# Performance work log

Measured on AMD Instinct MI355X. Metric: run time of the kernel, lower is better.

## Reference

```python
import jax, jax.numpy as jnp
import numpy as np

RADIUS = 8
EPS = 0.005

_DN = ('NCHW', 'OIHW', 'NCHW')

def _box_filter(t, r):
    """Separable normalized box filter with reflect padding. t: [H, W]."""
    ks = 2 * r + 1
    tp = jnp.pad(t, ((r, r), (r, r)), mode='reflect')[None, None]  # [1,1,H+2r,W+2r]
    kh = jnp.ones((1, 1, 1, ks), t.dtype) / ks
    kv = jnp.ones((1, 1, ks, 1), t.dtype) / ks
    out = jax.lax.conv_general_dilated(tp, kh, (1, 1), 'VALID', dimension_numbers=_DN)
    out = jax.lax.conv_general_dilated(out, kv, (1, 1), 'VALID', dimension_numbers=_DN)
    return out[0, 0]  # [H, W]

def setup_inputs() -> dict:
    key = jax.random.key(0)
    x = jax.random.uniform(key, (4096, 4096, 3), dtype=jnp.float32)
    return {"x": x}

def reference(x):
    # Rec.709 luma
    Y = 0.2126 * x[..., 0] + 0.7152 * x[..., 1] + 0.0722 * x[..., 2]  # [H,W]
    mean_I = _box_filter(Y, RADIUS)
    mean_II = _box_filter(Y * Y, RADIUS)
    var_I = mean_II - mean_I * mean_I
    a = var_I / (var_I + EPS)
    b = mean_I - a * mean_I
    mean_a = _box_filter(a, RADIUS)
    mean_b = _box_filter(b, RADIUS)
    Y_smooth = mean_a * Y + mean_b
    scale = (Y_smooth / jnp.maximum(Y, 1e-6))[..., None]  # [H,W,1]
    return jnp.clip(x * scale, 0.0, 1.0)
```

## Files before the change

### kernel.cpp

```cpp
#include <hip/hip_runtime.h>
#include <hip/hip_fp16.h>


#define HH 4096
#define WW 4096
#define TW 32
#define TH 64
#define SW 64
#define SH 96
#define SYS 65
#define HIS 49
#define HAS 33
#define INV289 (1.0f / 289.0f)
#define EPSV 0.005f

__device__ __forceinline__ int reflect_idx(int i, int n) {
    i = (i < 0) ? -i : i;
    i = (i >= n) ? (2 * n - 2 - i) : i;
    return i;
}

__global__ __launch_bounds__(256, 4) void gf_fused(const float* __restrict__ x,
                                                   float* __restrict__ out) {
    __shared__ __align__(16) char smem[15680 + 18816];
    __half*  sY    = (__half*)smem;
    __half2* ab    = (__half2*)smem;
    __half2* hIhII = (__half2*)(smem + 15680);
    __half2* hAhB  = (__half2*)(smem + 15680);

    const int t = threadIdx.x;
    const int tx = blockIdx.x * TW;
    const int ty = blockIdx.y * TH;

    {
        const int c  = t & 63;
        const int r0 = t >> 6;
        const bool interior = (tx >= 16) & (tx + 48 <= WW) & (ty >= 16) & (ty + 80 <= HH);
        if (interior) {
            const float* p = x + ((long)(ty + r0 - 16) * WW + (tx + c - 16)) * 3;
            for (int r = r0; r < SH; r += 4, p += 4 * WW * 3) {
                float Yv = 0.2126f * p[0] + 0.7152f * p[1] + 0.0722f * p[2];
                sY[r * SYS + c] = __float2half_rn(Yv);
            }
        } else {
            const int gx = reflect_idx(tx + c - 16, WW);
            for (int r = r0; r < SH; r += 4) {
                int gy = reflect_idx(ty + r - 16, HH);
                const float* p = x + ((long)gy * WW + gx) * 3;
                float Yv = 0.2126f * p[0] + 0.7152f * p[1] + 0.0722f * p[2];
                sY[r * SYS + c] = __float2half_rn(Yv);
            }
        }
    }
    __syncthreads();

    for (int task = t; task < SH * 3; task += 256) {
        int r = task % SH;
        int s = task / SH;
        int base = r * SYS + s * 16;
        int ob = r * HIS + s * 16;
        float sI = 0.f, sII = 0.f;
        #pragma unroll
        for (int k = 0; k <= 16; ++k) {
            float w = __half2float(sY[base + k]);
            sI += w; sII += w * w;
        }
        hIhII[ob] = __floats2half2_rn(sI, sII);
        #pragma unroll
        for (int j = 1; j < 16; ++j) {
            float va = __half2float(sY[base + 16 + j]);
            float vs = __half2float(sY[base + j - 1]);
            sI  += va - vs;
            sII += va * va - vs * vs;
            hIhII[ob + j] = __floats2half2_rn(sI, sII);
        }
    }
    __syncthreads();

    if (t < 240) {
        int c = t % 48;
        int q = t / 48;
        int r0 = q * 16;
        float sI = 0.f, sII = 0.f;
        #pragma unroll
        for (int k = 0; k <= 16; ++k) {
            float2 v = __half22float2(hIhII[(r0 + k) * HIS + c]);
            sI += v.x; sII += v.y;
        }
        #pragma unroll
        for (int j = 0; j < 16; ++j) {
            int o = r0 + j;
            float mI = sI * INV289;
            float mII = sII * INV289;
            float var = mII - mI * mI;
            float a = var / (var + EPSV);
            float b = mI - a * mI;
            ab[o * HIS + c] = __floats2half2_rn(a, b);
            if (j < 15) {
                float2 va = __half22float2(hIhII[(o + 17) * HIS + c]);
                float2 vs = __half22float2(hIhII[o * HIS + c]);
                sI  += va.x - vs.x;
                sII += va.y - vs.y;
            }
        }
    }
    __syncthreads();

    if (t < 160) {
        int r = t % 80;
        int s = t / 80;
        int base = r * HIS + s * 16;
        int ob = r * HAS + s * 16;
        float sA = 0.f, sB = 0.f;
        #pragma unroll
        for (int k = 0; k <= 16; ++k) {
            float2 v = __half22float2(ab[base + k]);
            sA += v.x; sB += v.y;
        }
        hAhB[ob] = __floats2half2_rn(sA, sB);
        #pragma unroll
        for (int j = 1; j < 16; ++j) {
            float2 va = __half22float2(ab[base + 16 + j]);
            float2 vs = __half22float2(ab[base + j - 1]);
            sA += va.x - vs.x;
            sB += va.y - vs.y;
            hAhB[ob + j] = __floats2half2_rn(sA, sB);
        }
    }
    __syncthreads();

    {
        int c = t & 31;
        int q = t >> 5;
        int r0 = q * 8;
        float sA = 0.f, sB = 0.f;
        #pragma unroll
        for (int k = 0; k <= 16; ++k) {
            float2 v = __half22float2(hAhB[(r0 + k) * HAS + c]);
            sA += v.x; sB += v.y;
        }
        #pragma unroll
        for (int j = 0; j < 8; ++j) {
            int o = r0 + j;
            float ma = sA * INV289;
            float mb = sB * INV289;
            int gy = ty + o, gx = tx + c;
            const float* p = x + ((long)gy * WW + gx) * 3;
            float rr = p[0], gg = p[1], bb = p[2];
            float Y = 0.2126f * rr + 0.7152f * gg + 0.0722f * bb;
            float scale = (ma * Y + mb) / fmaxf(Y, 1e-6f);
            float* qo = out + ((long)gy * WW + gx) * 3;
            qo[0] = fminf(fmaxf(rr * scale, 0.f), 1.f);
            qo[1] = fminf(fmaxf(gg * scale, 0.f), 1.f);
            qo[2] = fminf(fmaxf(bb * scale, 0.f), 1.f);
            if (j < 7) {
                float2 va = __half22float2(hAhB[(o + 17) * HAS + c]);
                float2 vs = __half22float2(hAhB[o * HAS + c]);
                sA += va.x - vs.x;
                sB += va.y - vs.y;
            }
        }
    }
}

extern "C" void kernel_launch(void* const* d_in, const int* in_sizes, int n_in,
                              void* d_out, int out_size, void* d_ws, size_t ws_size,
                              hipStream_t stream) {
    const float* x = (const float*)d_in[0];
    float* out = (float*)d_out;
    dim3 grid(WW / TW, HH / TH);
    gf_fused<<<grid, 256, 0, stream>>>(x, out);
}
```

Before: 397.2 us.

## Widen tiles to 64x64 with 512 threads, vectorize loads and stores

Doubles the tile width to 64 columns and the block size to 512 threads, which cuts the relative halo overhead (96x96 loaded per 64x64 output instead of 64x96 per 32x64). Global loads of RGB are vectorized as three float4 per four pixels. Output stores use float4 nontemporal stores, and two divisions are replaced with hardware reciprocal approximations. The cost is more shared memory per block and fewer blocks per CU, and the rcp approximation slightly changes numerics.

```diff
diff --git a/kernel.cpp b/kernel.cpp
--- a/kernel.cpp
+++ b/kernel.cpp
@@ -4,15 +4,20 @@
 
 #define HH 4096
 #define WW 4096
-#define TW 32
+#define TW 64
 #define TH 64
-#define SW 64
+#define SW 96
 #define SH 96
-#define SYS 65
-#define HIS 49
-#define HAS 33
+#define SYS 98
+#define HIS 81
+#define HAS 65
 #define INV289 (1.0f / 289.0f)
 #define EPSV 0.005f
+
+#define R1BYTES 25920
+#define R2BYTES 31104
+
+typedef float f32x4 __attribute__((ext_vector_type(4)));
 
 __device__ __forceinline__ int reflect_idx(int i, int n) {
     i = (i < 0) ? -i : i;
@@ -20,43 +25,55 @@
     return i;
 }
 
-__global__ __launch_bounds__(256, 4) void gf_fused(const float* __restrict__ x,
+__global__ __launch_bounds__(512, 4) void gf_fused(const float* __restrict__ x,
                                                    float* __restrict__ out) {
-    __shared__ __align__(16) char smem[15680 + 18816];
+    __shared__ __align__(16) char smem[R1BYTES + R2BYTES];
     __half*  sY    = (__half*)smem;
     __half2* ab    = (__half2*)smem;
-    __half2* hIhII = (__half2*)(smem + 15680);
-    __half2* hAhB  = (__half2*)(smem + 15680);
+    __half2* hIhII = (__half2*)(smem + R1BYTES);
+    __half2* hAhB  = (__half2*)(smem + R1BYTES);
 
     const int t = threadIdx.x;
     const int tx = blockIdx.x * TW;
     const int ty = blockIdx.y * TH;
 
     {
-        const int c  = t & 63;
-        const int r0 = t >> 6;
-        const bool interior = (tx >= 16) & (tx + 48 <= WW) & (ty >= 16) & (ty + 80 <= HH);
+        const bool interior = (tx >= 16) & (tx + SW - 16 <= WW) &
+                              (ty >= 16) & (ty + SH - 16 <= HH);
         if (interior) {
-            const float* p = x + ((long)(ty + r0 - 16) * WW + (tx + c - 16)) * 3;
-            for (int r = r0; r < SH; r += 4, p += 4 * WW * 3) {
-                float Yv = 0.2126f * p[0] + 0.7152f * p[1] + 0.0722f * p[2];
-                sY[r * SYS + c] = __float2half_rn(Yv);
+            for (int task = t; task < SH * 24; task += 512) {
+                int r = task / 24;
+                int g = task - r * 24;
+                const float4* p = (const float4*)(x + ((long)(ty + r - 16) * WW + (tx - 16 + 4 * g)) * 3);
+                float4 f0 = p[0], f1 = p[1], f2 = p[2];
+                float Y0 = 0.2126f * f0.x + 0.7152f * f0.y + 0.0722f * f0.z;
+                float Y1 = 0.2126f * f0.w + 0.7152f * f1.x + 0.0722f * f1.y;
+                float Y2 = 0.2126f * f1.z + 0.7152f * f1.w + 0.0722f * f2.x;
+                float Y3 = 0.2126f * f2.y + 0.7152f * f2.z + 0.0722f * f2.w;
+                __half2* q2 = (__half2*)&sY[r * SYS + 4 * g];
+                q2[0] = __floats2half2_rn(Y0, Y1);
+                q2[1] = __floats2half2_rn(Y2, Y3);
             }
         } else {
-            const int gx = reflect_idx(tx + c - 16, WW);
-            for (int r = r0; r < SH; r += 4) {
+            for (int task = t; task < SH * 24; task += 512) {
+                int r = task / 24;
+                int g = task - r * 24;
                 int gy = reflect_idx(ty + r - 16, HH);
-                const float* p = x + ((long)gy * WW + gx) * 3;
-                float Yv = 0.2126f * p[0] + 0.7152f * p[1] + 0.0722f * p[2];
-                sY[r * SYS + c] = __float2half_rn(Yv);
-            }
-        }
-    }
-    __syncthreads();
-
-    for (int task = t; task < SH * 3; task += 256) {
-        int r = task % SH;
-        int s = task / SH;
+                #pragma unroll
+                for (int cc = 0; cc < 4; ++cc) {
+                    int gx = reflect_idx(tx - 16 + 4 * g + cc, WW);
+                    const float* p = x + ((long)gy * WW + gx) * 3;
+                    float Yv = 0.2126f * p[0] + 0.7152f * p[1] + 0.0722f * p[2];
+                    sY[r * SYS + 4 * g + cc] = __float2half_rn(Yv);
+                }
+            }
+        }
+    }
+    __syncthreads();
+
+    if (t < 480) {
+        int r = t % 96;
+        int s = t / 96;
         int base = r * SYS + s * 16;
         int ob = r * HIS + s * 16;
         float sI = 0.f, sII = 0.f;
@@ -77,9 +94,9 @@
     }
     __syncthreads();
 
-    if (t < 240) {
-        int c = t % 48;
-        int q = t / 48;
+    if (t < 400) {
+        int c = t % 80;
+        int q = t / 80;
         int r0 = q * 16;
         float sI = 0.f, sII = 0.f;
         #pragma unroll
@@ -93,7 +110,7 @@
             float mI = sI * INV289;
             float mII = sII * INV289;
             float var = mII - mI * mI;
-            float a = var / (var + EPSV);
+            float a = var * __builtin_amdgcn_rcpf(var + EPSV);
             float b = mI - a * mI;
             ab[o * HIS + c] = __floats2half2_rn(a, b);
             if (j < 15) {
@@ -106,7 +123,7 @@
     }
     __syncthreads();
 
-    if (t < 160) {
+    if (t < 320) {
         int r = t % 80;
         int s = t / 80;
         int base = r * HIS + s * 16;
@@ -130,34 +147,56 @@
     __syncthreads();
 
     {
-        int c = t & 31;
-        int q = t >> 5;
-        int r0 = q * 8;
-        float sA = 0.f, sB = 0.f;
-        #pragma unroll
-        for (int k = 0; k <= 16; ++k) {
-            float2 v = __half22float2(hAhB[(r0 + k) * HAS + c]);
-            sA += v.x; sB += v.y;
-        }
-        #pragma unroll
-        for (int j = 0; j < 8; ++j) {
+        const int m  = t & 15;
+        const int q  = t >> 4;
+        const int r0 = q * 2;
+        const int c0 = m * 4;
+        float sA[4] = {0.f, 0.f, 0.f, 0.f};
+        float sB[4] = {0.f, 0.f, 0.f, 0.f};
+        #pragma unroll
+        for (int k = 0; k <= 16; ++k) {
+            int rb = (r0 + k) * HAS + c0;
+            #pragma unroll
+            for (int cc = 0; cc < 4; ++cc) {
+                float2 v = __half22float2(hAhB[rb + cc]);
+                sA[cc] += v.x; sB[cc] += v.y;
+            }
+        }
+        #pragma unroll
+        for (int j = 0; j < 2; ++j) {
             int o = r0 + j;
-            float ma = sA * INV289;
-            float mb = sB * INV289;
-            int gy = ty + o, gx = tx + c;
-            const float* p = x + ((long)gy * WW + gx) * 3;
-            float rr = p[0], gg = p[1], bb = p[2];
-            float Y = 0.2126f * rr + 0.7152f * gg + 0.0722f * bb;
-            float scale = (ma * Y + mb) / fmaxf(Y, 1e-6f);
-            float* qo = out + ((long)gy * WW + gx) * 3;
-            qo[0] = fminf(fmaxf(rr * scale, 0.f), 1.f);
-            qo[1] = fminf(fmaxf(gg * scale, 0.f), 1.f);
-            qo[2] = fminf(fmaxf(bb * scale, 0.f), 1.f);
-            if (j < 7) {
-                float2 va = __half22float2(hAhB[(o + 17) * HAS + c]);
-                float2 vs = __half22float2(hAhB[o * HAS + c]);
-                sA += va.x - vs.x;
-                sB += va.y - vs.y;
+            long gbase = ((long)(ty + o) * WW + (tx + c0)) * 3;
+            const float4* p = (const float4*)(x + gbase);
+            float4 f0 = p[0], f1 = p[1], f2 = p[2];
+            float px[12] = {f0.x, f0.y, f0.z, f0.w, f1.x, f1.y,
+                            f1.z, f1.w, f2.x, f2.y, f2.z, f2.w};
+            float ov[12];
+            #pragma unroll
+            for (int cc = 0; cc < 4; ++cc) {
+                float rr = px[3 * cc], gg = px[3 * cc + 1], bb = px[3 * cc + 2];
+                float Y = 0.2126f * rr + 0.7152f * gg + 0.0722f * bb;
+                float ma = sA[cc] * INV289;
+                float mb = sB[cc] * INV289;
+                float scale = (ma * Y + mb) * __builtin_amdgcn_rcpf(fmaxf(Y, 1e-6f));
+                ov[3 * cc]     = fminf(fmaxf(rr * scale, 0.f), 1.f);
+                ov[3 * cc + 1] = fminf(fmaxf(gg * scale, 0.f), 1.f);
+                ov[3 * cc + 2] = fminf(fmaxf(bb * scale, 0.f), 1.f);
+            }
+            f32x4* qo = (f32x4*)(out + gbase);
+            f32x4 s0 = {ov[0], ov[1], ov[2],  ov[3]};
+            f32x4 s1 = {ov[4], ov[5], ov[6],  ov[7]};
+            f32x4 s2 = {ov[8], ov[9], ov[10], ov[11]};
+            __builtin_nontemporal_store(s0, qo);
+            __builtin_nontemporal_store(s1, qo + 1);
+            __builtin_nontemporal_store(s2, qo + 2);
+            if (j == 0) {
+                #pragma unroll
+                for (int cc = 0; cc < 4; ++cc) {
+                    float2 va = __half22float2(hAhB[(o + 17) * HAS + c0 + cc]);
+                    float2 vs = __half22float2(hAhB[o * HAS + c0 + cc]);
+                    sA[cc] += va.x - vs.x;
+                    sB[cc] += va.y - vs.y;
+                }
             }
         }
     }
@@ -169,5 +208,5 @@
     const float* x = (const float*)d_in[0];
     float* out = (float*)d_out;
     dim3 grid(WW / TW, HH / TH);
-    gf_fused<<<grid, 256, 0, stream>>>(x, out);
+    gf_fused<<<grid, 512, 0, stream>>>(x, out);
 }
```

Result: faster. 358.3 us (-9.8%).
